# Performance work log

Hardware: AMD Instinct MI355X
Metric: run time of the kernel (lower is better)

The kernel has to match this reference:

```python
import jax, jax.numpy as jnp
import numpy as np

N_ITERS = 10
OMEGA = 10
W_HALF = 512          # hpm.W
D = 2 * W_HALF        # real-lifted signal dim
BATCH = 4096
P_PREV = 8
EPS = 1e-8


def hard_thr(x, omega=OMEGA):
    # x: [B, D]; keep the omega largest-|x| entries per row, zero the rest
    # (equivalent to torch scatter-zero of the D-omega smallest |x|)
    _, idx = jax.lax.top_k(jnp.abs(x), omega)            # [B, omega]
    rows = jnp.arange(x.shape[0])[:, None]
    mask = jnp.zeros_like(x).at[rows, idx].set(1.0)
    return x * mask


def _spectral_density(z):
    # z: [B, D] -> squared complex magnitude summed over batch, min-max normalized
    w = z.shape[1] // 2
    p = z[:, :w] ** 2 + z[:, w:] ** 2                    # [B, W] (sign flip of imag part cancels)
    mD = p.sum(0)                                        # [W]
    return (mD - mD.min()) / (mD.max() - mD.min() + EPS)


def setup_inputs() -> dict:
    key = jax.random.key(0)
    k0, k1, k2 = jax.random.split(key, 3)
    x = jax.random.normal(k0, (BATCH, D), jnp.float32)
    prev_windows = jax.random.normal(k1, (P_PREV, BATCH, D), jnp.float32)
    # learned dictionary (stand-in for the real-lifted partial Fourier matrix)
    W_d = jax.random.normal(k2, (1, D, D), jnp.float32) / np.sqrt(D).astype(np.float32)
    L = jnp.float32(5.0)                                 # hpm.L (fixed Lipschitz constant)
    S = jnp.eye(D, dtype=jnp.float32)[None] - (1.0 / L) * jnp.matmul(
        jnp.swapaxes(W_d, 1, 2), W_d)                    # [1, D, D]
    lambda2 = jnp.float32(1.0)
    return {"x": x, "prev_windows": prev_windows, "W_d": W_d, "S": S,
            "lambda2": lambda2, "L": L}


def reference(x, prev_windows, W_d, S, lambda2, L):
    Wd0 = W_d[0]                                         # [D, D]
    S0 = S[0]                                            # [D, D]
    w = D // 2

    # B = (1/L * W_d) @ x   (column-vector matvec as row GEMM)
    b = (x @ Wd0.T) / L                                  # [B, D]

    # two warm-up ISTA/IHT steps
    z = hard_thr(b)
    c = b + z @ S0.T
    z = hard_thr(c)

    mD_normalized = _spectral_density(z)                 # [W]

    # ---- attention over previous windows (prev_windows non-empty branch) ----
    pw = prev_windows                                    # [P, B, D]
    p_prev = pw[:, :, :w] ** 2 + pw[:, :, w:] ** 2       # [P, B, W]
    mD_prev = p_prev.sum(1)                              # [P, W]
    mn = mD_prev.min(axis=1, keepdims=True)
    mx = mD_prev.max(axis=1, keepdims=True)
    prev_mDn = (mD_prev - mn) / (mx - mn + EPS)          # [P, W]

    att = prev_mDn @ mD_normalized[:, None]              # [P, 1]
    att = jax.nn.softmax(att / np.sqrt(float(w)).astype(np.float32), axis=0)
    pw_clamped = jnp.clip(pw, -150.0, 150.0)
    z = (pw_clamped * att[:, None]).sum(0) * lambda2     # [B, D]

    # ---- unrolled iterations ----
    for _ in range(N_ITERS):
        c = b + z @ S0.T
        z = hard_thr(c)

    mD_normalized = _spectral_density(z)                 # [W]
    return (mD_normalized, z)
```

## Files before the change

### kernel.cpp

```cpp
#include <hip/hip_runtime.h>
#include <stdint.h>

#define BATCH 4096
#define DIM   1024
#define PPREV 8
#define CAP   128

__device__ __forceinline__ int lt_count(unsigned long long m) {
    return __builtin_amdgcn_mbcnt_hi((unsigned)(m >> 32),
           __builtin_amdgcn_mbcnt_lo((unsigned)m, 0));
}
__device__ __forceinline__ bool kp_gt(int ak, int ap, int bk, int bp) {
    return (ak > bk) || (ak == bk && ap > bp);
}

template<bool SEEDED>
__device__ __forceinline__ void select10_block(
    const float cz[4], int tid, int lane, int wid,
    int2* s_cand, int2* s_win, int* s_cnt, int2* s_red, int* s_bnd,
    int& tbits, int wi[10], float wv[10])
{
    int k[4], pay[4];
    #pragma unroll
    for (int t = 0; t < 4; ++t) {
        int bb = __float_as_int(cz[t]);
        k[t]   = bb & 0x7fffffff;
        pay[t] = ((1023 - (tid * 4 + t)) << 1) | (int)((unsigned)bb >> 31);
    }

    if (!SEEDED) {
        int lm = max(max(k[0], k[1]), max(k[2], k[3]));
        #pragma unroll
        for (int k2 = 2; k2 <= 64; k2 <<= 1) {
            #pragma unroll
            for (int j = k2 >> 1; j > 0; j >>= 1) {
                int p = __shfl_xor(lm, j);
                bool keep_max = (((lane & k2) == 0) == ((lane & j) == 0));
                if ((p > lm) == keep_max) lm = p;
            }
        }
        int wb = __builtin_amdgcn_readlane(lm, 9);
        if (lane == 0) s_bnd[wid] = wb;
        __syncthreads();
        tbits = max(max(s_bnd[0], s_bnd[1]), max(s_bnd[2], s_bnd[3]));
    }

    int tb = tbits;
    #pragma unroll 1
    for (;;) {
        unsigned long long b0 = __ballot(k[0] >= tb);
        unsigned long long b1 = __ballot(k[1] >= tb);
        unsigned long long b2 = __ballot(k[2] >= tb);
        unsigned long long b3 = __ballot(k[3] >= tb);
        int wcnt = __popcll(b0) + __popcll(b1) + __popcll(b2) + __popcll(b3);
        if (lane == 0) s_cnt[wid] = wcnt;
        __syncthreads();
        const int c0 = s_cnt[0], c1 = s_cnt[1], c2 = s_cnt[2], c3 = s_cnt[3];
        const int total = c0 + c1 + c2 + c3;
        __syncthreads();

        if (total >= 10) {
            if (total <= CAP) {
                int off = (wid > 0 ? c0 : 0) + (wid > 1 ? c1 : 0) + (wid > 2 ? c2 : 0);
                int o0 = off + lt_count(b0);  off += __popcll(b0);
                int o1 = off + lt_count(b1);  off += __popcll(b1);
                int o2 = off + lt_count(b2);  off += __popcll(b2);
                int o3 = off + lt_count(b3);
                if (k[0] >= tb) s_cand[o0] = make_int2(k[0], pay[0]);
                if (k[1] >= tb) s_cand[o1] = make_int2(k[1], pay[1]);
                if (k[2] >= tb) s_cand[o2] = make_int2(k[2], pay[2]);
                if (k[3] >= tb) s_cand[o3] = make_int2(k[3], pay[3]);
                __syncthreads();
                if (tid < total) {
                    int2 mine = s_cand[tid];
                    int rank = 0, e = 0;
                    #pragma unroll 1
                    for (; e + 4 <= total; e += 4) {
                        int2 q0 = s_cand[e], q1 = s_cand[e+1], q2 = s_cand[e+2], q3 = s_cand[e+3];
                        rank += kp_gt(q0.x, q0.y, mine.x, mine.y) ? 1 : 0;
                        rank += kp_gt(q1.x, q1.y, mine.x, mine.y) ? 1 : 0;
                        rank += kp_gt(q2.x, q2.y, mine.x, mine.y) ? 1 : 0;
                        rank += kp_gt(q3.x, q3.y, mine.x, mine.y) ? 1 : 0;
                    }
                    #pragma unroll 1
                    for (; e < total; ++e) {
                        int2 q = s_cand[e];
                        rank += kp_gt(q.x, q.y, mine.x, mine.y) ? 1 : 0;
                    }
                    if (rank < 10) s_win[rank] = mine;
                }
                __syncthreads();
            } else {
                #pragma unroll 1
                for (int r = 0; r < 10; ++r) {
                    int bk = k[0], bp = pay[0];
                    #pragma unroll
                    for (int t = 1; t < 4; ++t)
                        if (kp_gt(k[t], pay[t], bk, bp)) { bk = k[t]; bp = pay[t]; }
                    #pragma unroll
                    for (int m = 1; m < 64; m <<= 1) {
                        int ok = __shfl_xor(bk, m), op = __shfl_xor(bp, m);
                        if (kp_gt(ok, op, bk, bp)) { bk = ok; bp = op; }
                    }
                    if (lane == 0) s_red[wid] = make_int2(bk, bp);
                    __syncthreads();
                    if (tid == 0) {
                        int2 best = s_red[0];
                        #pragma unroll
                        for (int w2 = 1; w2 < 4; ++w2) {
                            int2 cc = s_red[w2];
                            if (kp_gt(cc.x, cc.y, best.x, best.y)) best = cc;
                        }
                        s_win[r] = best;
                    }
                    __syncthreads();
                    int2 wr = s_win[r];
                    #pragma unroll
                    for (int t = 0; t < 4; ++t)
                        if (k[t] == wr.x && pay[t] == wr.y) k[t] = -1;
                }
            }
            break;
        }
        tb = (tb > 0x00800000) ? (tb - 0x00800000) : 0;
    }

    #pragma unroll
    for (int r = 0; r < 10; ++r) {
        int2 wr = s_win[r];
        wi[r] = 1023 - (wr.y >> 1);
        wv[r] = __int_as_float(wr.x | ((wr.y & 1) << 31));
    }
    tbits = __float_as_int(wv[9]) & 0x7fffffff;
}

__device__ __forceinline__ void gather_block(const float bz[4], float cz[4],
                                             const float* __restrict__ S,
                                             const int wi[10], const float wv[10], int tid)
{
    #pragma unroll
    for (int t = 0; t < 4; ++t) cz[t] = bz[t];
    #pragma unroll
    for (int kk = 0; kk < 10; ++kk) {
        int row = __builtin_amdgcn_readfirstlane(wi[kk]);
        const float wvs = wv[kk];
        float4 v = *(const float4*)(S + (size_t)row * DIM + tid * 4);
        cz[0] += wvs * v.x;
        cz[1] += wvs * v.y;
        cz[2] += wvs * v.z;
        cz[3] += wvs * v.w;
    }
}

__global__ __launch_bounds__(256)
void warmup_rows(const float* __restrict__ b, const float* __restrict__ S,
                 int* __restrict__ sidx, float* __restrict__ sval)
{
    __shared__ int2 s_cand[CAP];
    __shared__ int2 s_win[10];
    __shared__ int2 s_red[4];
    __shared__ int  s_cnt[4];
    __shared__ int  s_bnd[4];
    const int tid = threadIdx.x, lane = tid & 63, wid = tid >> 6;
    const int r = blockIdx.x;
    float4 bv = *(const float4*)(b + (size_t)r * DIM + tid * 4);
    float bz[4] = {bv.x, bv.y, bv.z, bv.w};
    int wi[10]; float wv[10]; int tbits = 0;
    select10_block<false>(bz, tid, lane, wid, s_cand, s_win, s_cnt, s_red, s_bnd, tbits, wi, wv);
    float cz[4];
    gather_block(bz, cz, S, wi, wv, tid);
    select10_block<true>(cz, tid, lane, wid, s_cand, s_win, s_cnt, s_red, s_bnd, tbits, wi, wv);
    if (tid < 10) {
        int2 wr = s_win[tid];
        sidx[r * 10 + tid] = 1023 - (wr.y >> 1);
        sval[r * 10 + tid] = __int_as_float(wr.x | ((wr.y & 1) << 31));
    }
}

__global__ __launch_bounds__(256)
void loop_rows(const float* __restrict__ c1, const float* __restrict__ b,
               const float* __restrict__ S, float* __restrict__ zout,
               int* __restrict__ sidx, float* __restrict__ sval)
{
    __shared__ int2 s_cand[CAP];
    __shared__ int2 s_win[10];
    __shared__ int2 s_red[4];
    __shared__ int  s_cnt[4];
    __shared__ int  s_bnd[4];
    const int tid = threadIdx.x, lane = tid & 63, wid = tid >> 6;
    const int r = blockIdx.x;
    float4 bv = *(const float4*)(b  + (size_t)r * DIM + tid * 4);
    float4 cv = *(const float4*)(c1 + (size_t)r * DIM + tid * 4);
    float bz[4] = {bv.x, bv.y, bv.z, bv.w};
    float cz[4] = {cv.x, cv.y, cv.z, cv.w};
    int wi[10]; float wv[10]; int tbits = 0;
    select10_block<false>(cz, tid, lane, wid, s_cand, s_win, s_cnt, s_red, s_bnd, tbits, wi, wv);
    int pwi[10], pwb[10];
    #pragma unroll 1
    for (int it = 0; it < 9; ++it) {
        #pragma unroll
        for (int kk = 0; kk < 10; ++kk) { pwi[kk] = wi[kk]; pwb[kk] = __float_as_int(wv[kk]); }
        gather_block(bz, cz, S, wi, wv, tid);
        select10_block<true>(cz, tid, lane, wid, s_cand, s_win, s_cnt, s_red, s_bnd, tbits, wi, wv);
        bool same = true;
        #pragma unroll
        for (int kk = 0; kk < 10; ++kk)
            same = same && (wi[kk] == pwi[kk]) && (__float_as_int(wv[kk]) == pwb[kk]);
        if (same) break;
    }
    float e[4];
    #pragma unroll
    for (int t = 0; t < 4; ++t) {
        const int j = tid * 4 + t;
        float v = 0.0f;
        #pragma unroll
        for (int kk = 0; kk < 10; ++kk) v = (wi[kk] == j) ? wv[kk] : v;
        e[t] = v;
    }
    float4 o; o.x = e[0]; o.y = e[1]; o.z = e[2]; o.w = e[3];
    *(float4*)(zout + (size_t)r * DIM + tid * 4) = o;
    if (tid < 10) {
        int2 wr = s_win[tid];
        sidx[r * 10 + tid] = 1023 - (wr.y >> 1);
        sval[r * 10 + tid] = __int_as_float(wr.x | ((wr.y & 1) << 31));
    }
}

template<bool DIV_L, bool HAS_ADD>
__global__ __launch_bounds__(256)
void gemm_f32(const float* __restrict__ A, const float* __restrict__ B,
              const float* __restrict__ addM, float* __restrict__ C,
              const float* __restrict__ Lptr, int M, int N, int K)
{
    __shared__ float As[16][132];
    __shared__ float Bs[16][68];
    const int tid = threadIdx.x;
    const int m0 = blockIdx.y * 128, n0 = blockIdx.x * 64;
    const int ty = tid >> 4, tx = tid & 15;
    const int sarow = tid >> 1;
    const int sak   = (tid & 1) * 8;
    const int sbrow = tid >> 2;
    const int sbk   = (tid & 3) * 4;
    float acc[8][4] = {};
    const float* Ab = A + (size_t)(m0 + sarow) * K + sak;
    const float* Bb = B + (size_t)(n0 + sbrow) * K + sbk;
    float4 av0 = *(const float4*)(Ab);
    float4 av1 = *(const float4*)(Ab + 4);
    float4 bv0 = *(const float4*)(Bb);
    for (int k0 = 0; k0 < K; k0 += 16) {
        __syncthreads();
        As[sak+0][sarow] = av0.x; As[sak+1][sarow] = av0.y; As[sak+2][sarow] = av0.z; As[sak+3][sarow] = av0.w;
        As[sak+4][sarow] = av1.x; As[sak+5][sarow] = av1.y; As[sak+6][sarow] = av1.z; As[sak+7][sarow] = av1.w;
        Bs[sbk+0][sbrow] = bv0.x; Bs[sbk+1][sbrow] = bv0.y; Bs[sbk+2][sbrow] = bv0.z; Bs[sbk+3][sbrow] = bv0.w;
        __syncthreads();
        if (k0 + 16 < K) {
            av0 = *(const float4*)(Ab + k0 + 16);
            av1 = *(const float4*)(Ab + k0 + 20);
            bv0 = *(const float4*)(Bb + k0 + 16);
        }
        #pragma unroll
        for (int k = 0; k < 16; ++k) {
            float4 a40 = *(const float4*)&As[k][ty*8];
            float4 a41 = *(const float4*)&As[k][ty*8+4];
            float4 b40 = *(const float4*)&Bs[k][tx*4];
            float am[8] = {a40.x,a40.y,a40.z,a40.w,a41.x,a41.y,a41.z,a41.w};
            float bn[4] = {b40.x,b40.y,b40.z,b40.w};
            #pragma unroll
            for (int i = 0; i < 8; ++i)
                #pragma unroll
                for (int j = 0; j < 4; ++j)
                    acc[i][j] += am[i] * bn[j];
        }
    }
    const float invL = DIV_L ? (1.0f / *Lptr) : 1.0f;
    #pragma unroll
    for (int i = 0; i < 8; ++i) {
        size_t row = (size_t)(m0 + ty*8 + i);
        float4 rv; 
        rv.x = acc[i][0]; rv.y = acc[i][1]; rv.z = acc[i][2]; rv.w = acc[i][3];
        if (DIV_L) { rv.x *= invL; rv.y *= invL; rv.z *= invL; rv.w *= invL; }
        if (HAS_ADD) {
            float4 ad = *(const float4*)(addM + row * N + n0 + tx*4);
            rv.x += ad.x; rv.y += ad.y; rv.z += ad.z; rv.w += ad.w;
        }
        *(float4*)(C + row * N + n0 + tx*4) = rv;
    }
}

__global__ void sparse_density_stage1(const int* __restrict__ sidx,
                                      const float* __restrict__ sval,
                                      float* __restrict__ partial)
{
    const int w = threadIdx.x;
    const int blk = blockIdx.x;
    const int base = blk * 64 * 10;
    float acc = 0.0f;
    for (int e = 0; e < 640; ++e) {
        int d = sidx[base + e];
        float v = sval[base + e];
        if ((d & 511) == w) acc += v * v;
    }
    partial[blk * 512 + w] = acc;
}

__global__ void prev_density_stage1(const float* __restrict__ pw, float* __restrict__ partial)
{
    const int p = blockIdx.x, chunk = blockIdx.y;
    const int w = threadIdx.x;
    const float* base = pw + ((size_t)p * BATCH + (size_t)chunk * 64) * DIM;
    float acc = 0.0f;
    for (int i = 0; i < 64; ++i) {
        float a = base[(size_t)i * DIM + w];
        float c = base[(size_t)i * DIM + 512 + w];
        acc += a * a + c * c;
    }
    partial[((size_t)(p * 64 + chunk)) * 512 + w] = acc;
}

__global__ void prev_density_stage2(const float* __restrict__ partial, float* __restrict__ mD_prev)
{
    const int p = blockIdx.x; const int w = threadIdx.x;
    float acc = 0.0f;
    for (int i = 0; i < 64; ++i) acc += partial[((size_t)(p * 64 + i)) * 512 + w];
    mD_prev[p * 512 + w] = acc;
}

__device__ __forceinline__ float wave_fmax(float v) {
    #pragma unroll
    for (int m = 1; m < 64; m <<= 1) v = fmaxf(v, __shfl_xor(v, m));
    return v;
}
__device__ __forceinline__ float wave_fmin(float v) {
    #pragma unroll
    for (int m = 1; m < 64; m <<= 1) v = fminf(v, __shfl_xor(v, m));
    return v;
}
__device__ __forceinline__ float wave_fsum(float v) {
    #pragma unroll
    for (int m = 1; m < 64; m <<= 1) v += __shfl_xor(v, m);
    return v;
}

__global__ void density2_attention(const float* __restrict__ partial,
                                   const float* __restrict__ mD_prev,
                                   float* __restrict__ att)
{
    __shared__ float md1[512];
    __shared__ float att_l[PPREV];
    const int tid = threadIdx.x, lane = tid & 63, w = tid >> 6;
    float v = 0.0f;
    for (int i = 0; i < 64; ++i) v += partial[i * 512 + tid];
    md1[tid] = v;
    __syncthreads();
    float t8[8], u8[8];
    {
        const float4* m4 = (const float4*)(&md1[lane * 8]);
        float4 a = m4[0], bq = m4[1];
        t8[0]=a.x; t8[1]=a.y; t8[2]=a.z; t8[3]=a.w; t8[4]=bq.x; t8[5]=bq.y; t8[6]=bq.z; t8[7]=bq.w;
        const float4* p4 = (const float4*)(mD_prev + w * 512 + lane * 8);
        float4 c = p4[0], d = p4[1];
        u8[0]=c.x; u8[1]=c.y; u8[2]=c.z; u8[3]=c.w; u8[4]=d.x; u8[5]=d.y; u8[6]=d.z; u8[7]=d.w;
    }
    float mx = t8[0], mn = t8[0], pmx = u8[0], pmn = u8[0];
    #pragma unroll
    for (int i = 1; i < 8; ++i) {
        mx = fmaxf(mx, t8[i]); mn = fminf(mn, t8[i]);
        pmx = fmaxf(pmx, u8[i]); pmn = fminf(pmn, u8[i]);
    }
    mx = wave_fmax(mx); mn = wave_fmin(mn);
    pmx = wave_fmax(pmx); pmn = wave_fmin(pmn);
    const float inv  = 1.0f / (mx - mn + 1e-8f);
    const float pinv = 1.0f / (pmx - pmn + 1e-8f);
    float dot = 0.0f;
    #pragma unroll
    for (int i = 0; i < 8; ++i) dot += ((u8[i] - pmn) * pinv) * ((t8[i] - mn) * inv);
    dot = wave_fsum(dot);
    if (lane == 0) att_l[w] = dot / 22.627417f;
    __syncthreads();
    if (tid == 0) {
        float m = att_l[0];
        #pragma unroll
        for (int p = 1; p < PPREV; ++p) m = fmaxf(m, att_l[p]);
        float e[PPREV], s = 0.0f;
        #pragma unroll
        for (int p = 0; p < PPREV; ++p) { e[p] = expf(att_l[p] - m); s += e[p]; }
        #pragma unroll
        for (int p = 0; p < PPREV; ++p) att[p] = e[p] / s;
    }
}

__global__ __launch_bounds__(256)
void weighted_sum(const float* __restrict__ pw, const float* __restrict__ att,
                  const float* __restrict__ lam, float* __restrict__ zatt)
{
    const size_t i = ((size_t)blockIdx.x * 256 + threadIdx.x) * 4;
    const float l2 = *lam;
    float a[PPREV];
    #pragma unroll
    for (int p = 0; p < PPREV; ++p) a[p] = att[p];
    float4 acc = make_float4(0.f, 0.f, 0.f, 0.f);
    #pragma unroll
    for (int p = 0; p < PPREV; ++p) {
        float4 v = *(const float4*)(pw + (size_t)p * BATCH * DIM + i);
        v.x = fminf(fmaxf(v.x, -150.f), 150.f);
        v.y = fminf(fmaxf(v.y, -150.f), 150.f);
        v.z = fminf(fmaxf(v.z, -150.f), 150.f);
        v.w = fminf(fmaxf(v.w, -150.f), 150.f);
        acc.x += v.x * a[p]; acc.y += v.y * a[p]; acc.z += v.z * a[p]; acc.w += v.w * a[p];
    }
    acc.x *= l2; acc.y *= l2; acc.z *= l2; acc.w *= l2;
    *(float4*)(zatt + i) = acc;
}

__global__ void finalize_fused(const float* __restrict__ partial, float* __restrict__ out)
{
    __shared__ float red[512];
    const int tid = threadIdx.x;
    float v = 0.0f;
    for (int i = 0; i < 64; ++i) v += partial[i * 512 + tid];
    red[tid] = v; __syncthreads();
    for (int off = 256; off > 0; off >>= 1) { if (tid < off) red[tid] = fmaxf(red[tid], red[tid+off]); __syncthreads(); }
    float mx = red[0]; __syncthreads();
    red[tid] = v; __syncthreads();
    for (int off = 256; off > 0; off >>= 1) { if (tid < off) red[tid] = fminf(red[tid], red[tid+off]); __syncthreads(); }
    float mn = red[0];
    out[tid] = (v - mn) / (mx - mn + 1e-8f);
}

extern "C" void kernel_launch(void* const* d_in, const int* in_sizes, int n_in,
                              void* d_out, int out_size, void* d_ws, size_t ws_size,
                              hipStream_t stream)
{
    const float* x   = (const float*)d_in[0];
    const float* pw  = (const float*)d_in[1];
    const float* Wd  = (const float*)d_in[2];
    const float* S   = (const float*)d_in[3];
    const float* lam = (const float*)d_in[4];
    const float* L   = (const float*)d_in[5];
    float* out = (float*)d_out;

    float* b       = (float*)d_ws;
    float* zatt    = b + (size_t)BATCH * DIM;
    float* pp_prev = zatt + (size_t)BATCH * DIM;
    float* pp_dens = pp_prev + 262144;
    float* mD_prev = pp_dens + 32768;
    float* attw    = mD_prev + 4096;
    float* sval1   = attw + 8;
    float* sval2   = sval1 + 40960;
    int*   sidx1   = (int*)(sval2 + 40960);
    int*   sidx2   = sidx1 + 40960;

    float* c1   = out + 512;
    float* zout = out + 512;

    const dim3 gg(DIM / 64, BATCH / 128);

    gemm_f32<true,  false><<<gg, 256, 0, stream>>>(x, Wd, nullptr, b, L, BATCH, DIM, DIM);
    warmup_rows<<<BATCH, 256, 0, stream>>>(b, S, sidx1, sval1);
    sparse_density_stage1<<<64, 512, 0, stream>>>(sidx1, sval1, pp_dens);
    prev_density_stage1<<<dim3(PPREV, 64), 512, 0, stream>>>(pw, pp_prev);
    prev_density_stage2<<<PPREV, 512, 0, stream>>>(pp_prev, mD_prev);
    density2_attention<<<1, 512, 0, stream>>>(pp_dens, mD_prev, attw);
    weighted_sum<<<(BATCH * DIM) / 1024, 256, 0, stream>>>(pw, attw, lam, zatt);
    gemm_f32<false, true ><<<gg, 256, 0, stream>>>(zatt, S, b, c1, nullptr, BATCH, DIM, DIM);
    loop_rows<<<BATCH, 256, 0, stream>>>(c1, b, S, zout, sidx2, sval2);
    sparse_density_stage1<<<64, 512, 0, stream>>>(sidx2, sval2, pp_dens);
    finalize_fused<<<1, 512, 0, stream>>>(pp_dens, out);
}
```

Before: 527.3 us.

## Double-buffer 128x128 FP32 GEMM and fuse candidate compaction into threshold loop

The two dense GEMMs now use a 128x128 tile with an 8x8 per-thread micro-tile and double-buffered shared memory, so each step needs one barrier instead of two and each thread gets more register reuse. The top-10 selection writes candidates into per-wave buckets during the threshold-lowering loop itself, which drops the separate compaction pass and one barrier per iteration. If any wave overflows its bucket, it falls back to iterative max reduction. The trade-offs are higher register and LDS use per block, which may reduce occupancy, and half as many GEMM blocks.

```diff
diff --git a/kernel.cpp b/kernel.cpp
--- a/kernel.cpp
+++ b/kernel.cpp
@@ -4,7 +4,7 @@
 #define BATCH 4096
 #define DIM   1024
 #define PPREV 8
-#define CAP   128
+#define CAPW  64
 
 __device__ __forceinline__ int lt_count(unsigned long long m) {
     return __builtin_amdgcn_mbcnt_hi((unsigned)(m >> 32),
@@ -15,9 +15,9 @@
 }
 
 template<bool SEEDED>
-__device__ __forceinline__ void select10_block(
+__device__ __forceinline__ void select10_blk(
     const float cz[4], int tid, int lane, int wid,
-    int2* s_cand, int2* s_win, int* s_cnt, int2* s_red, int* s_bnd,
+    int2 (*s_cand)[CAPW], int2* s_win, int* s_cnt, int2* s_red, int* s_bnd,
     int& tbits, int wi[10], float wv[10])
 {
     int k[4], pay[4];
@@ -46,83 +46,96 @@
     }
 
     int tb = tbits;
+    int c0, c1, c2, c3, total; bool bad;
     #pragma unroll 1
     for (;;) {
         unsigned long long b0 = __ballot(k[0] >= tb);
         unsigned long long b1 = __ballot(k[1] >= tb);
         unsigned long long b2 = __ballot(k[2] >= tb);
         unsigned long long b3 = __ballot(k[3] >= tb);
-        int wcnt = __popcll(b0) + __popcll(b1) + __popcll(b2) + __popcll(b3);
-        if (lane == 0) s_cnt[wid] = wcnt;
+        int pos = lt_count(b0);
+        if (k[0] >= tb && pos < CAPW) s_cand[wid][pos] = make_int2(k[0], pay[0]);
+        int base = __popcll(b0);
+        pos = base + lt_count(b1);
+        if (k[1] >= tb && pos < CAPW) s_cand[wid][pos] = make_int2(k[1], pay[1]);
+        base += __popcll(b1);
+        pos = base + lt_count(b2);
+        if (k[2] >= tb && pos < CAPW) s_cand[wid][pos] = make_int2(k[2], pay[2]);
+        base += __popcll(b2);
+        pos = base + lt_count(b3);
+        if (k[3] >= tb && pos < CAPW) s_cand[wid][pos] = make_int2(k[3], pay[3]);
+        base += __popcll(b3);
+        if (lane == 0) s_cnt[wid] = base;
         __syncthreads();
-        const int c0 = s_cnt[0], c1 = s_cnt[1], c2 = s_cnt[2], c3 = s_cnt[3];
-        const int total = c0 + c1 + c2 + c3;
+        c0 = s_cnt[0]; c1 = s_cnt[1]; c2 = s_cnt[2]; c3 = s_cnt[3];
+        total = c0 + c1 + c2 + c3;
+        bad = (c0 > CAPW) || (c1 > CAPW) || (c2 > CAPW) || (c3 > CAPW);
+        if (total >= 10 || tb == 0) break;
+        tb = (tb > 0x00800000) ? (tb - 0x00800000) : 0;
         __syncthreads();
-
-        if (total >= 10) {
-            if (total <= CAP) {
-                int off = (wid > 0 ? c0 : 0) + (wid > 1 ? c1 : 0) + (wid > 2 ? c2 : 0);
-                int o0 = off + lt_count(b0);  off += __popcll(b0);
-                int o1 = off + lt_count(b1);  off += __popcll(b1);
-                int o2 = off + lt_count(b2);  off += __popcll(b2);
-                int o3 = off + lt_count(b3);
-                if (k[0] >= tb) s_cand[o0] = make_int2(k[0], pay[0]);
-                if (k[1] >= tb) s_cand[o1] = make_int2(k[1], pay[1]);
-                if (k[2] >= tb) s_cand[o2] = make_int2(k[2], pay[2]);
-                if (k[3] >= tb) s_cand[o3] = make_int2(k[3], pay[3]);
-                __syncthreads();
-                if (tid < total) {
-                    int2 mine = s_cand[tid];
-                    int rank = 0, e = 0;
-                    #pragma unroll 1
-                    for (; e + 4 <= total; e += 4) {
-                        int2 q0 = s_cand[e], q1 = s_cand[e+1], q2 = s_cand[e+2], q3 = s_cand[e+3];
-                        rank += kp_gt(q0.x, q0.y, mine.x, mine.y) ? 1 : 0;
-                        rank += kp_gt(q1.x, q1.y, mine.x, mine.y) ? 1 : 0;
-                        rank += kp_gt(q2.x, q2.y, mine.x, mine.y) ? 1 : 0;
-                        rank += kp_gt(q3.x, q3.y, mine.x, mine.y) ? 1 : 0;
-                    }
-                    #pragma unroll 1
-                    for (; e < total; ++e) {
-                        int2 q = s_cand[e];
-                        rank += kp_gt(q.x, q.y, mine.x, mine.y) ? 1 : 0;
-                    }
-                    if (rank < 10) s_win[rank] = mine;
+    }
+
+    if (!bad) {
+        if (tid < total) {
+            int w, e;
+            if      (tid < c0)           { w = 0; e = tid; }
+            else if (tid < c0 + c1)      { w = 1; e = tid - c0; }
+            else if (tid < c0 + c1 + c2) { w = 2; e = tid - c0 - c1; }
+            else                         { w = 3; e = tid - c0 - c1 - c2; }
+            int2 mine = s_cand[w][e];
+            int cns[4] = {c0, c1, c2, c3};
+            int rank = 0;
+            #pragma unroll
+            for (int w2 = 0; w2 < 4; ++w2) {
+                const int cn = cns[w2];
+                const int2* reg = s_cand[w2];
+                int e2 = 0;
+                #pragma unroll 1
+                for (; e2 + 4 <= cn; e2 += 4) {
+                    int2 q0 = reg[e2], q1 = reg[e2+1], q2 = reg[e2+2], q3 = reg[e2+3];
+                    rank += kp_gt(q0.x, q0.y, mine.x, mine.y) ? 1 : 0;
+                    rank += kp_gt(q1.x, q1.y, mine.x, mine.y) ? 1 : 0;
+                    rank += kp_gt(q2.x, q2.y, mine.x, mine.y) ? 1 : 0;
+                    rank += kp_gt(q3.x, q3.y, mine.x, mine.y) ? 1 : 0;
                 }
-                __syncthreads();
-            } else {
                 #pragma unroll 1
-                for (int r = 0; r < 10; ++r) {
-                    int bk = k[0], bp = pay[0];
-                    #pragma unroll
-                    for (int t = 1; t < 4; ++t)
-                        if (kp_gt(k[t], pay[t], bk, bp)) { bk = k[t]; bp = pay[t]; }
-                    #pragma unroll
-                    for (int m = 1; m < 64; m <<= 1) {
-                        int ok = __shfl_xor(bk, m), op = __shfl_xor(bp, m);
-                        if (kp_gt(ok, op, bk, bp)) { bk = ok; bp = op; }
-                    }
-                    if (lane == 0) s_red[wid] = make_int2(bk, bp);
-                    __syncthreads();
-                    if (tid == 0) {
-                        int2 best = s_red[0];
-                        #pragma unroll
-                        for (int w2 = 1; w2 < 4; ++w2) {
-                            int2 cc = s_red[w2];
-                            if (kp_gt(cc.x, cc.y, best.x, best.y)) best = cc;
-                        }
-                        s_win[r] = best;
-                    }
-                    __syncthreads();
-                    int2 wr = s_win[r];
-                    #pragma unroll
-                    for (int t = 0; t < 4; ++t)
-                        if (k[t] == wr.x && pay[t] == wr.y) k[t] = -1;
+                for (; e2 < cn; ++e2) {
+                    int2 q = reg[e2];
+                    rank += kp_gt(q.x, q.y, mine.x, mine.y) ? 1 : 0;
                 }
             }
-            break;
-        }
-        tb = (tb > 0x00800000) ? (tb - 0x00800000) : 0;
+            if (rank < 10) s_win[rank] = mine;
+        }
+        __syncthreads();
+    } else {
+        #pragma unroll 1
+        for (int r = 0; r < 10; ++r) {
+            int bk = k[0], bp = pay[0];
+            #pragma unroll
+            for (int t = 1; t < 4; ++t)
+                if (kp_gt(k[t], pay[t], bk, bp)) { bk = k[t]; bp = pay[t]; }
+            #pragma unroll
+            for (int m = 1; m < 64; m <<= 1) {
+                int ok = __shfl_xor(bk, m), op = __shfl_xor(bp, m);
+                if (kp_gt(ok, op, bk, bp)) { bk = ok; bp = op; }
+            }
+            if (lane == 0) s_red[wid] = make_int2(bk, bp);
+            __syncthreads();
+            if (tid == 0) {
+                int2 best = s_red[0];
+                #pragma unroll
+                for (int w2 = 1; w2 < 4; ++w2) {
+                    int2 cc = s_red[w2];
+                    if (kp_gt(cc.x, cc.y, best.x, best.y)) best = cc;
+                }
+                s_win[r] = best;
+            }
+            __syncthreads();
+            int2 wr = s_win[r];
+            #pragma unroll
+            for (int t = 0; t < 4; ++t)
+                if (k[t] == wr.x && pay[t] == wr.y) k[t] = -1;
+        }
     }
 
     #pragma unroll
@@ -156,7 +169,7 @@
 void warmup_rows(const float* __restrict__ b, const float* __restrict__ S,
                  int* __restrict__ sidx, float* __restrict__ sval)
 {
-    __shared__ int2 s_cand[CAP];
+    __shared__ int2 s_cand[4][CAPW];
     __shared__ int2 s_win[10];
     __shared__ int2 s_red[4];
     __shared__ int  s_cnt[4];
@@ -166,10 +179,10 @@
     float4 bv = *(const float4*)(b + (size_t)r * DIM + tid * 4);
     float bz[4] = {bv.x, bv.y, bv.z, bv.w};
     int wi[10]; float wv[10]; int tbits = 0;
-    select10_block<false>(bz, tid, lane, wid, s_cand, s_win, s_cnt, s_red, s_bnd, tbits, wi, wv);
+    select10_blk<false>(bz, tid, lane, wid, s_cand, s_win, s_cnt, s_red, s_bnd, tbits, wi, wv);
     float cz[4];
     gather_block(bz, cz, S, wi, wv, tid);
-    select10_block<true>(cz, tid, lane, wid, s_cand, s_win, s_cnt, s_red, s_bnd, tbits, wi, wv);
+    select10_blk<true>(cz, tid, lane, wid, s_cand, s_win, s_cnt, s_red, s_bnd, tbits, wi, wv);
     if (tid < 10) {
         int2 wr = s_win[tid];
         sidx[r * 10 + tid] = 1023 - (wr.y >> 1);
@@ -182,7 +195,7 @@
                const float* __restrict__ S, float* __restrict__ zout,
                int* __restrict__ sidx, float* __restrict__ sval)
 {
-    __shared__ int2 s_cand[CAP];
+    __shared__ int2 s_cand[4][CAPW];
     __shared__ int2 s_win[10];
     __shared__ int2 s_red[4];
     __shared__ int  s_cnt[4];
@@ -194,14 +207,14 @@
     float bz[4] = {bv.x, bv.y, bv.z, bv.w};
     float cz[4] = {cv.x, cv.y, cv.z, cv.w};
     int wi[10]; float wv[10]; int tbits = 0;
-    select10_block<false>(cz, tid, lane, wid, s_cand, s_win, s_cnt, s_red, s_bnd, tbits, wi, wv);
+    select10_blk<false>(cz, tid, lane, wid, s_cand, s_win, s_cnt, s_red, s_bnd, tbits, wi, wv);
     int pwi[10], pwb[10];
     #pragma unroll 1
     for (int it = 0; it < 9; ++it) {
         #pragma unroll
         for (int kk = 0; kk < 10; ++kk) { pwi[kk] = wi[kk]; pwb[kk] = __float_as_int(wv[kk]); }
         gather_block(bz, cz, S, wi, wv, tid);
-        select10_block<true>(cz, tid, lane, wid, s_cand, s_win, s_cnt, s_red, s_bnd, tbits, wi, wv);
+        select10_blk<true>(cz, tid, lane, wid, s_cand, s_win, s_cnt, s_red, s_bnd, tbits, wi, wv);
         bool same = true;
         #pragma unroll
         for (int kk = 0; kk < 10; ++kk)
@@ -228,62 +241,93 @@
 
 template<bool DIV_L, bool HAS_ADD>
 __global__ __launch_bounds__(256)
-void gemm_f32(const float* __restrict__ A, const float* __restrict__ B,
-              const float* __restrict__ addM, float* __restrict__ C,
-              const float* __restrict__ Lptr, int M, int N, int K)
-{
-    __shared__ float As[16][132];
-    __shared__ float Bs[16][68];
+void gemm_dbuf(const float* __restrict__ A, const float* __restrict__ B,
+               const float* __restrict__ addM, float* __restrict__ C,
+               const float* __restrict__ Lptr, int M, int N, int K)
+{
+    __shared__ __align__(16) float As[2][16][132];
+    __shared__ __align__(16) float Bs[2][16][132];
     const int tid = threadIdx.x;
-    const int m0 = blockIdx.y * 128, n0 = blockIdx.x * 64;
+    const int m0 = blockIdx.y * 128, n0 = blockIdx.x * 128;
     const int ty = tid >> 4, tx = tid & 15;
-    const int sarow = tid >> 1;
-    const int sak   = (tid & 1) * 8;
-    const int sbrow = tid >> 2;
-    const int sbk   = (tid & 3) * 4;
-    float acc[8][4] = {};
-    const float* Ab = A + (size_t)(m0 + sarow) * K + sak;
-    const float* Bb = B + (size_t)(n0 + sbrow) * K + sbk;
-    float4 av0 = *(const float4*)(Ab);
-    float4 av1 = *(const float4*)(Ab + 4);
-    float4 bv0 = *(const float4*)(Bb);
-    for (int k0 = 0; k0 < K; k0 += 16) {
-        __syncthreads();
-        As[sak+0][sarow] = av0.x; As[sak+1][sarow] = av0.y; As[sak+2][sarow] = av0.z; As[sak+3][sarow] = av0.w;
-        As[sak+4][sarow] = av1.x; As[sak+5][sarow] = av1.y; As[sak+6][sarow] = av1.z; As[sak+7][sarow] = av1.w;
-        Bs[sbk+0][sbrow] = bv0.x; Bs[sbk+1][sbrow] = bv0.y; Bs[sbk+2][sbrow] = bv0.z; Bs[sbk+3][sbrow] = bv0.w;
-        __syncthreads();
-        if (k0 + 16 < K) {
-            av0 = *(const float4*)(Ab + k0 + 16);
-            av1 = *(const float4*)(Ab + k0 + 20);
-            bv0 = *(const float4*)(Bb + k0 + 16);
+    const int srow = tid >> 1;
+    const int sk   = (tid & 1) * 8;
+    float acc[8][8] = {};
+    const float* Ab = A + (size_t)(m0 + srow) * K + sk;
+    const float* Bb = B + (size_t)(n0 + srow) * K + sk;
+
+    float4 ra0 = *(const float4*)(Ab);
+    float4 ra1 = *(const float4*)(Ab + 4);
+    float4 rb0 = *(const float4*)(Bb);
+    float4 rb1 = *(const float4*)(Bb + 4);
+
+    const int NT = K / 16;
+    {
+        float* ap = &As[0][sk][srow];
+        ap[0*132]=ra0.x; ap[1*132]=ra0.y; ap[2*132]=ra0.z; ap[3*132]=ra0.w;
+        ap[4*132]=ra1.x; ap[5*132]=ra1.y; ap[6*132]=ra1.z; ap[7*132]=ra1.w;
+        float* bp = &Bs[0][sk][srow];
+        bp[0*132]=rb0.x; bp[1*132]=rb0.y; bp[2*132]=rb0.z; bp[3*132]=rb0.w;
+        bp[4*132]=rb1.x; bp[5*132]=rb1.y; bp[6*132]=rb1.z; bp[7*132]=rb1.w;
+    }
+    __syncthreads();
+
+    #pragma unroll 1
+    for (int t = 0; t < NT; ++t) {
+        const int cur = t & 1;
+        if (t + 1 < NT) {
+            const int ko = (t + 1) * 16;
+            ra0 = *(const float4*)(Ab + ko);
+            ra1 = *(const float4*)(Ab + ko + 4);
+            rb0 = *(const float4*)(Bb + ko);
+            rb1 = *(const float4*)(Bb + ko + 4);
         }
         #pragma unroll
         for (int k = 0; k < 16; ++k) {
-            float4 a40 = *(const float4*)&As[k][ty*8];
-            float4 a41 = *(const float4*)&As[k][ty*8+4];
-            float4 b40 = *(const float4*)&Bs[k][tx*4];
+            float4 a40 = *(const float4*)&As[cur][k][ty*8];
+            float4 a41 = *(const float4*)&As[cur][k][ty*8+4];
+            float4 b40 = *(const float4*)&Bs[cur][k][tx*8];
+            float4 b41 = *(const float4*)&Bs[cur][k][tx*8+4];
             float am[8] = {a40.x,a40.y,a40.z,a40.w,a41.x,a41.y,a41.z,a41.w};
-            float bn[4] = {b40.x,b40.y,b40.z,b40.w};
+            float bn[8] = {b40.x,b40.y,b40.z,b40.w,b41.x,b41.y,b41.z,b41.w};
             #pragma unroll
             for (int i = 0; i < 8; ++i)
                 #pragma unroll
-                for (int j = 0; j < 4; ++j)
+                for (int j = 0; j < 8; ++j)
                     acc[i][j] += am[i] * bn[j];
         }
-    }
+        if (t + 1 < NT) {
+            const int nxt = (t + 1) & 1;
+            float* ap = &As[nxt][sk][srow];
+            ap[0*132]=ra0.x; ap[1*132]=ra0.y; ap[2*132]=ra0.z; ap[3*132]=ra0.w;
+            ap[4*132]=ra1.x; ap[5*132]=ra1.y; ap[6*132]=ra1.z; ap[7*132]=ra1.w;
+            float* bp = &Bs[nxt][sk][srow];
+            bp[0*132]=rb0.x; bp[1*132]=rb0.y; bp[2*132]=rb0.z; bp[3*132]=rb0.w;
+            bp[4*132]=rb1.x; bp[5*132]=rb1.y; bp[6*132]=rb1.z; bp[7*132]=rb1.w;
+            __syncthreads();
+        }
+    }
+
     const float invL = DIV_L ? (1.0f / *Lptr) : 1.0f;
     #pragma unroll
     for (int i = 0; i < 8; ++i) {
         size_t row = (size_t)(m0 + ty*8 + i);
-        float4 rv; 
-        rv.x = acc[i][0]; rv.y = acc[i][1]; rv.z = acc[i][2]; rv.w = acc[i][3];
-        if (DIV_L) { rv.x *= invL; rv.y *= invL; rv.z *= invL; rv.w *= invL; }
+        float* Cp = C + row * N + n0 + tx*8;
+        float4 r0, r1;
+        r0.x=acc[i][0]; r0.y=acc[i][1]; r0.z=acc[i][2]; r0.w=acc[i][3];
+        r1.x=acc[i][4]; r1.y=acc[i][5]; r1.z=acc[i][6]; r1.w=acc[i][7];
+        if (DIV_L) {
+            r0.x*=invL; r0.y*=invL; r0.z*=invL; r0.w*=invL;
+            r1.x*=invL; r1.y*=invL; r1.z*=invL; r1.w*=invL;
+        }
         if (HAS_ADD) {
-            float4 ad = *(const float4*)(addM + row * N + n0 + tx*4);
-            rv.x += ad.x; rv.y += ad.y; rv.z += ad.z; rv.w += ad.w;
-        }
-        *(float4*)(C + row * N + n0 + tx*4) = rv;
+            float4 a0 = *(const float4*)(addM + row * N + n0 + tx*8);
+            float4 a1 = *(const float4*)(addM + row * N + n0 + tx*8 + 4);
+            r0.x+=a0.x; r0.y+=a0.y; r0.z+=a0.z; r0.w+=a0.w;
+            r1.x+=a1.x; r1.y+=a1.y; r1.z+=a1.z; r1.w+=a1.w;
+        }
+        *(float4*)(Cp)     = r0;
+        *(float4*)(Cp + 4) = r1;
     }
 }
 
@@ -453,16 +497,16 @@
     float* c1   = out + 512;
     float* zout = out + 512;
 
-    const dim3 gg(DIM / 64, BATCH / 128);
-
-    gemm_f32<true,  false><<<gg, 256, 0, stream>>>(x, Wd, nullptr, b, L, BATCH, DIM, DIM);
+    const dim3 gg(DIM / 128, BATCH / 128);
+
+    gemm_dbuf<true,  false><<<gg, 256, 0, stream>>>(x, Wd, nullptr, b, L, BATCH, DIM, DIM);
     warmup_rows<<<BATCH, 256, 0, stream>>>(b, S, sidx1, sval1);
     sparse_density_stage1<<<64, 512, 0, stream>>>(sidx1, sval1, pp_dens);
     prev_density_stage1<<<dim3(PPREV, 64), 512, 0, stream>>>(pw, pp_prev);
     prev_density_stage2<<<PPREV, 512, 0, stream>>>(pp_prev, mD_prev);
     density2_attention<<<1, 512, 0, stream>>>(pp_dens, mD_prev, attw);
     weighted_sum<<<(BATCH * DIM) / 1024, 256, 0, stream>>>(pw, attw, lam, zatt);
-    gemm_f32<false, true ><<<gg, 256, 0, stream>>>(zatt, S, b, c1, nullptr, BATCH, DIM, DIM);
+    gemm_dbuf<false, true ><<<gg, 256, 0, stream>>>(zatt, S, b, c1, nullptr, BATCH, DIM, DIM);
     loop_rows<<<BATCH, 256, 0, stream>>>(c1, b, S, zout, sidx2, sval2);
     sparse_density_stage1<<<64, 512, 0, stream>>>(sidx2, sval2, pp_dens);
     finalize_fused<<<1, 512, 0, stream>>>(pp_dens, out);
```

Result: slower. 601.8 us (+14.1%).
